# Optimization experiments

Measured on AMD Instinct MI355X. Metric: run time of the kernel, lower is better.

Reference implementation:

```python
import jax, jax.numpy as jnp
import numpy as np

D, H1, O, E = 1024, 4096, 1024, 8
B = 8192


def setup_inputs() -> dict:
    key = jax.random.key(0)
    k1, k2, k3, k4 = jax.random.split(key, 4)
    # kaiming_uniform_ with nonlinearity='relu': bound = sqrt(6 / fan_in), fan_in = last dim
    b_w1 = float(np.sqrt(6.0 / D))
    b_w2 = float(np.sqrt(6.0 / H1))
    x = jax.random.normal(k1, (B, D), dtype=jnp.float32)
    eid = jax.random.randint(k2, (B,), 0, E, dtype=jnp.int32)
    W1 = jax.random.uniform(k3, (E, H1, D), dtype=jnp.float32, minval=-b_w1, maxval=b_w1)
    W2 = jax.random.uniform(k4, (E, O, H1), dtype=jnp.float32, minval=-b_w2, maxval=b_w2)
    b2 = jnp.zeros((E, O), dtype=jnp.float32)
    return {"x": x, "eid": eid, "W1": W1, "W2": W2, "b2": b2}


def reference(x, eid, W1, W2, b2):
    # Per-token expert MLP: y_i = gelu(x_i @ W1[eid_i].T) @ W2[eid_i].T + b2[eid_i]
    # Dense-dispatch formulation: loop over the (small, static) expert axis,
    # compute each expert MLP on all tokens, and select per-token via mask.
    # Math is identical to the sort/gather/scatter original.
    y = jnp.zeros((x.shape[0], W2.shape[1]), dtype=x.dtype)
    for e in range(W1.shape[0]):
        h = jax.nn.gelu(x @ W1[e].T, approximate=False)   # [B, H1]
        y_e = h @ W2[e].T + b2[e]                          # [B, O]
        mask = (eid == e)[:, None].astype(x.dtype)
        y = y + mask * y_e
    return y
```

## Files before the change

### kernel.cpp

```cpp
#include <hip/hip_runtime.h>
#include <hip/hip_bf16.h>
#include <math.h>

constexpr int kD  = 1024;
constexpr int kH1 = 4096;
constexpr int kO  = 1024;
constexpr int kE  = 8;
constexpr int kB  = 8192;

constexpr int BM   = 128;
constexpr int MAXT = kB / BM + kE;

typedef __attribute__((ext_vector_type(8))) short short8;
typedef __attribute__((ext_vector_type(4))) float f32x4;

__device__ __forceinline__ unsigned short f2bf(float f) {
  unsigned int u = __float_as_uint(f);
  u += 0x7fffu + ((u >> 16) & 1u);
  return (unsigned short)(u >> 16);
}
__device__ __forceinline__ float bf2f(unsigned short u) {
  return __uint_as_float(((unsigned int)u) << 16);
}

__device__ __forceinline__ float gelu_fast(float x) {
  float u = 0.7978845608028654f * (x + 0.044715f * x * x * x);
  float eu = __expf(2.0f * u);
  float th = 1.0f - 2.0f / (eu + 1.0f);
  return 0.5f * x * (1.0f + th);
}

__global__ __launch_bounds__(256) void setup_kernel(const int* __restrict__ eid,
                                                    int* __restrict__ perm,
                                                    int* __restrict__ tiles) {
  __shared__ int cnt[kE];
  __shared__ int off[kE];
  __shared__ int cur[kE];
  int t = threadIdx.x;
  if (t < kE) { cnt[t] = 0; cur[t] = 0; }
  __syncthreads();
  for (int i = t; i < kB; i += 256) atomicAdd(&cnt[eid[i]], 1);
  __syncthreads();
  if (t == 0) {
    int o = 0, nt = 0;
    for (int e = 0; e < kE; ++e) {
      off[e] = o;
      int c = cnt[e];
      for (int r = 0; r < c; r += BM) {
        tiles[nt * 4 + 0] = e;
        tiles[nt * 4 + 1] = o + r;
        tiles[nt * 4 + 2] = (c - r < BM) ? (c - r) : BM;
        tiles[nt * 4 + 3] = 0;
        ++nt;
      }
      o += c;
    }
    for (; nt < MAXT; ++nt) {
      tiles[nt * 4 + 0] = 0; tiles[nt * 4 + 1] = 0;
      tiles[nt * 4 + 2] = 0; tiles[nt * 4 + 3] = 0;
    }
  }
  __syncthreads();
  for (int i = t; i < kB; i += 256) {
    int e = eid[i];
    int p = off[e] + atomicAdd(&cur[e], 1);
    perm[p] = i;
  }
}

__global__ __launch_bounds__(256) void gather_kernel(const float* __restrict__ x,
                                                     const int* __restrict__ perm,
                                                     unsigned short* __restrict__ xg) {
  int idx = blockIdx.x * 256 + threadIdx.x;
  int pos = idx >> 7;
  int c   = (idx & 127) << 3;
  int row = perm[pos];
  const float4* s = (const float4*)(x + (size_t)row * kD + c);
  float4 f0 = s[0], f1 = s[1];
  short8 v;
  v[0] = (short)f2bf(f0.x); v[1] = (short)f2bf(f0.y);
  v[2] = (short)f2bf(f0.z); v[3] = (short)f2bf(f0.w);
  v[4] = (short)f2bf(f1.x); v[5] = (short)f2bf(f1.y);
  v[6] = (short)f2bf(f1.z); v[7] = (short)f2bf(f1.w);
  *(short8*)(xg + (size_t)pos * kD + c) = v;
}

__global__ __launch_bounds__(256) void convert_kernel(const float* __restrict__ src,
                                                      unsigned short* __restrict__ dst,
                                                      int n8) {
  int stride = gridDim.x * 256;
  for (int i = blockIdx.x * 256 + threadIdx.x; i < n8; i += stride) {
    const float4* s = (const float4*)(src + (size_t)i * 8);
    float4 f0 = s[0], f1 = s[1];
    short8 v;
    v[0] = (short)f2bf(f0.x); v[1] = (short)f2bf(f0.y);
    v[2] = (short)f2bf(f0.z); v[3] = (short)f2bf(f0.w);
    v[4] = (short)f2bf(f1.x); v[5] = (short)f2bf(f1.y);
    v[6] = (short)f2bf(f1.z); v[7] = (short)f2bf(f1.w);
    *(short8*)(dst + (size_t)i * 8) = v;
  }
}

template <int KTOT, int KTILES, int N, int NPAN, int MODE>
__global__ __launch_bounds__(512, 2) void gemm2p_kernel(
    const unsigned short* __restrict__ Amat,
    const unsigned short* __restrict__ Bmat,
    const int* __restrict__ tiles,
    const int* __restrict__ perm,
    unsigned short* __restrict__ out_bf,
    float* __restrict__ out_f) {
  extern __shared__ unsigned short lds[];

  constexpr int total = MAXT * NPAN;
  constexpr int cpx = total >> 3;
  constexpr int nchN = NPAN / 4;
  const int bid = blockIdx.x;
  const int id = (bid & 7) * cpx + (bid >> 3);
  const int chunk = id >> 4;
  const int a16 = id & 15;
  const int ti = (chunk / nchN) * 4 + (a16 & 3);
  const int pancol = (chunk % nchN) * 4 + (a16 >> 2);

  int n0, kb, half;
  if constexpr (MODE == 0) {
    n0 = pancol * 256; kb = 0; half = 0;
  } else {
    half = pancol >> 2; n0 = (pancol & 3) * 256; kb = half * (KTOT / 2);
  }

  const int e  = tiles[ti * 4 + 0];
  const int rs = tiles[ti * 4 + 1];
  const int nr = tiles[ti * 4 + 2];
  if (nr == 0) return;

  const int t = threadIdx.x;
  const int l = t & 63;
  const int w = t >> 6;
  const int r0 = (w >> 2) * 64;
  const int wc16 = (w & 3) * 16;

  const unsigned short* Bp = Bmat + (size_t)e * N * KTOT;

  int offA[4][2], offB[4][2];
#pragma unroll
  for (int mr = 0; mr < 4; ++mr)
#pragma unroll
    for (int ks = 0; ks < 2; ++ks) {
      int r = r0 + mr * 16 + (l & 15);
      offA[mr][ks] = r * 64 + ((ks * 32 + (l >> 4) * 8) ^ ((r & 7) << 3));
    }
#pragma unroll
  for (int j = 0; j < 4; ++j)
#pragma unroll
    for (int ks = 0; ks < 2; ++ks) {
      int rB = 64 * (j & 1) + wc16 + (l & 15);
      offB[j][ks] = (j >> 1) * 8192 + rB * 64 +
                    ((ks * 32 + (l >> 4) * 8) ^ ((rB & 7) << 3));
    }

  auto stage = [&](int buf, int k0, int idx) {
    const int slot = idx >> 1, hf = idx & 1;
    int elem = (hf * 512 + t) * 8;
    int r = elem >> 6, cp = elem & 63;
    int cl = cp ^ ((r & 7) << 3);
    const unsigned short* src =
        (slot == 0) ? Amat + (size_t)(rs + r) * KTOT + k0 + cl
                    : Bp + (size_t)(n0 + (slot - 1) * 128 + r) * KTOT + k0 + cl;
    unsigned short* dst = lds + buf * 24576 + slot * 8192 + elem;
    __builtin_amdgcn_global_load_lds(
        (const __attribute__((address_space(1))) unsigned int*)src,
        (__attribute__((address_space(3))) unsigned int*)dst, 16, 0, 0);
  };

  short8 aF[4][2], bF[4][2];
  f32x4 acc[4][4] = {};

  auto readA = [&](int buf) {
    const unsigned short* base = lds + buf * 24576;
#pragma unroll
    for (int mr = 0; mr < 4; ++mr)
#pragma unroll
      for (int ks = 0; ks < 2; ++ks)
        aF[mr][ks] = *(const short8*)(base + offA[mr][ks]);
  };
  auto readB = [&](int buf, int jlo) {
    const unsigned short* base = lds + buf * 24576 + 8192;
#pragma unroll
    for (int j = 0; j < 2; ++j)
#pragma unroll
      for (int ks = 0; ks < 2; ++ks)
        bF[jlo + j][ks] = *(const short8*)(base + offB[jlo + j][ks]);
  };
  auto mfmaH = [&](int jlo) {
    __builtin_amdgcn_s_setprio(1);
#pragma unroll
    for (int j = 0; j < 2; ++j)
#pragma unroll
      for (int mr = 0; mr < 4; ++mr)
#pragma unroll
        for (int ks = 0; ks < 2; ++ks)
          acc[jlo + j][mr] = __builtin_amdgcn_mfma_f32_16x16x32_bf16(
              aF[mr][ks], bF[jlo + j][ks], acc[jlo + j][mr], 0, 0, 0);
    __builtin_amdgcn_s_setprio(0);
  };

#pragma unroll
  for (int idx = 0; idx < 6; ++idx) stage(0, kb, idx);

  for (int kt = 0; kt < KTILES - 1; ++kt) {
    const int buf = kt & 1;
    const int nb = buf ^ 1;
    const int k0n = kb + (kt + 1) * 64;
    asm volatile("s_waitcnt vmcnt(2)" ::: "memory");
    __builtin_amdgcn_s_barrier();
    readA(buf);
    readB(buf, 0);
    stage(nb, k0n, 0); stage(nb, k0n, 1); stage(nb, k0n, 2);
    __builtin_amdgcn_s_barrier();
    mfmaH(0);
    asm volatile("s_waitcnt vmcnt(3)" ::: "memory");
    __builtin_amdgcn_s_barrier();
    readB(buf, 2);
    stage(nb, k0n, 3); stage(nb, k0n, 4); stage(nb, k0n, 5);
    __builtin_amdgcn_s_barrier();
    mfmaH(2);
  }
  {
    const int buf = (KTILES - 1) & 1;
    asm volatile("s_waitcnt vmcnt(2)" ::: "memory");
    __builtin_amdgcn_s_barrier();
    readA(buf);
    readB(buf, 0);
    __builtin_amdgcn_s_barrier();
    mfmaH(0);
    asm volatile("s_waitcnt vmcnt(0)" ::: "memory");
    __builtin_amdgcn_s_barrier();
    readB(buf, 2);
    __builtin_amdgcn_s_barrier();
    mfmaH(2);
  }

  const int lr4 = (l >> 4) * 4;
  const int lc  = l & 15;
#pragma unroll
  for (int mr = 0; mr < 4; ++mr)
#pragma unroll
    for (int rg = 0; rg < 4; ++rg) {
      int row = r0 + mr * 16 + lr4 + rg;
      if (row < nr) {
        if constexpr (MODE == 0) {
          unsigned short* dst = out_bf + (size_t)(rs + row) * N + n0;
#pragma unroll
          for (int j = 0; j < 4; ++j)
            dst[j * 64 + wc16 + lc] = f2bf(gelu_fast(acc[j][mr][rg]));
        } else {
          if (half == 0) {
            float* dst = out_f + (size_t)perm[rs + row] * N + n0;
#pragma unroll
            for (int j = 0; j < 4; ++j)
              dst[j * 64 + wc16 + lc] = acc[j][mr][rg];
          } else {
            unsigned short* dst = out_bf + (size_t)(rs + row) * N + n0;
#pragma unroll
            for (int j = 0; j < 4; ++j)
              dst[j * 64 + wc16 + lc] = f2bf(acc[j][mr][rg]);
          }
        }
      }
    }
}

__global__ __launch_bounds__(256) void reduce_kernel(float* __restrict__ y,
                                                     const unsigned short* __restrict__ part,
                                                     const int* __restrict__ perm,
                                                     const int* __restrict__ eid,
                                                     const float* __restrict__ b2) {
  int idx = blockIdx.x * 256 + threadIdx.x;
  int p = idx >> 7;
  int c = (idx & 127) << 3;
  int orig = perm[p];
  int e = eid[orig];
  float* yp = y + (size_t)orig * kO + c;
  short8 pv = *(const short8*)(part + (size_t)p * kO + c);
  const float* bp = b2 + (size_t)e * kO + c;
  float4 y0 = *(float4*)yp, y1 = *(float4*)(yp + 4);
  float4 b0 = *(const float4*)bp, b1 = *(const float4*)(bp + 4);
  y0.x += bf2f((unsigned short)pv[0]) + b0.x;
  y0.y += bf2f((unsigned short)pv[1]) + b0.y;
  y0.z += bf2f((unsigned short)pv[2]) + b0.z;
  y0.w += bf2f((unsigned short)pv[3]) + b0.w;
  y1.x += bf2f((unsigned short)pv[4]) + b1.x;
  y1.y += bf2f((unsigned short)pv[5]) + b1.y;
  y1.z += bf2f((unsigned short)pv[6]) + b1.z;
  y1.w += bf2f((unsigned short)pv[7]) + b1.w;
  *(float4*)yp = y0;
  *(float4*)(yp + 4) = y1;
}

extern "C" void kernel_launch(void* const* d_in, const int* in_sizes, int n_in,
                              void* d_out, int out_size, void* d_ws, size_t ws_size,
                              hipStream_t stream) {
  const float* x  = (const float*)d_in[0];
  const int*  eid = (const int*)d_in[1];
  const float* W1 = (const float*)d_in[2];
  const float* W2 = (const float*)d_in[3];
  const float* b2 = (const float*)d_in[4];
  float* y = (float*)d_out;

  char* ws = (char*)d_ws;
  int* perm  = (int*)ws;
  int* tiles = (int*)(ws + 32768);
  unsigned short* xg = (unsigned short*)(ws + 36864);
  size_t xg_bytes = (size_t)(kB + 256) * kD * 2;
  unsigned short* h  = (unsigned short*)(ws + 36864 + xg_bytes);
  size_t h_bytes = (size_t)(kB + 256) * kH1 * 2;
  unsigned short* Wb = (unsigned short*)(ws + 36864 + xg_bytes + h_bytes);

  constexpr int kWelems8 = kE * kH1 * kD / 8;

  auto g1 = gemm2p_kernel<kD, 16, kH1, 16, 0>;
  auto g2 = gemm2p_kernel<kH1, 32, kO, 8, 1>;
  hipFuncSetAttribute((const void*)g1, hipFuncAttributeMaxDynamicSharedMemorySize, 98304);
  hipFuncSetAttribute((const void*)g2, hipFuncAttributeMaxDynamicSharedMemorySize, 98304);

  setup_kernel<<<1, 256, 0, stream>>>(eid, perm, tiles);
  gather_kernel<<<(kB * kD / 8) / 256, 256, 0, stream>>>(x, perm, xg);

  convert_kernel<<<2048, 256, 0, stream>>>(W1, Wb, kWelems8);
  g1<<<MAXT * 16, 512, 98304, stream>>>(xg, Wb, tiles, perm, h, nullptr);

  convert_kernel<<<2048, 256, 0, stream>>>(W2, Wb, kWelems8);
  g2<<<MAXT * 8, 512, 98304, stream>>>(h, Wb, tiles, perm, xg, y);

  reduce_kernel<<<(kB * kO / 8) / 256, 256, 0, stream>>>(y, xg, perm, eid, b2);
}
```

Baseline: 340.4 us.

## Make expert GEMMs persistent with cross-tile prefetch of next tile's operands

Both grouped GEMM launches become persistent kernels on a fixed grid of 256 workgroups. Each workgroup loops over tiles with a stride of 256. During the last K-step of the current tile it stages the first K-slice of the next tile, so the load pipeline stays busy across tile boundaries and the per-block prologue is paid once per workgroup. In exchange, only one workgroup per CU is resident even though the launch bounds allow two. Empty padding tiles no longer exit early and run the full MMA loop, and tile counts that are not a multiple of 256 can leave a ragged tail.

```diff
diff --git a/kernel.cpp b/kernel.cpp
--- a/kernel.cpp
+++ b/kernel.cpp
@@ -102,7 +102,7 @@
 }
 
 template <int KTOT, int KTILES, int N, int NPAN, int MODE>
-__global__ __launch_bounds__(512, 2) void gemm2p_kernel(
+__global__ __launch_bounds__(512, 2) void gemmp_kernel(
     const unsigned short* __restrict__ Amat,
     const unsigned short* __restrict__ Bmat,
     const int* __restrict__ tiles,
@@ -110,36 +110,41 @@
     unsigned short* __restrict__ out_bf,
     float* __restrict__ out_f) {
   extern __shared__ unsigned short lds[];
-
-  constexpr int total = MAXT * NPAN;
-  constexpr int cpx = total >> 3;
-  constexpr int nchN = NPAN / 4;
+  constexpr int TOTAL = MAXT * NPAN;
+  constexpr int nchN = NPAN / 4 > 0 ? NPAN / 4 : 1;
+
   const int bid = blockIdx.x;
-  const int id = (bid & 7) * cpx + (bid >> 3);
-  const int chunk = id >> 4;
-  const int a16 = id & 15;
-  const int ti = (chunk / nchN) * 4 + (a16 & 3);
-  const int pancol = (chunk % nchN) * 4 + (a16 >> 2);
-
-  int n0, kb, half;
-  if constexpr (MODE == 0) {
-    n0 = pancol * 256; kb = 0; half = 0;
-  } else {
-    half = pancol >> 2; n0 = (pancol & 3) * 256; kb = half * (KTOT / 2);
-  }
-
-  const int e  = tiles[ti * 4 + 0];
-  const int rs = tiles[ti * 4 + 1];
-  const int nr = tiles[ti * 4 + 2];
-  if (nr == 0) return;
-
   const int t = threadIdx.x;
   const int l = t & 63;
   const int w = t >> 6;
   const int r0 = (w >> 2) * 64;
   const int wc16 = (w & 3) * 16;
 
-  const unsigned short* Bp = Bmat + (size_t)e * N * KTOT;
+  struct TP {
+    const unsigned short* Ab;
+    const unsigned short* Bb;
+    int rs, nr, n0, half;
+  };
+
+  auto mkTP = [&](int wg) {
+    TP p;
+    int id = (wg & 7) * (TOTAL / 8) + (wg >> 3);
+    int chunk = id >> 4, a16 = id & 15;
+    int ti = (chunk / nchN) * 4 + (a16 & 3);
+    int pancol = (chunk % nchN) * 4 + (a16 >> 2);
+    int kb;
+    if constexpr (MODE == 0) {
+      p.n0 = pancol * 256; kb = 0; p.half = 0;
+    } else {
+      p.half = pancol >> 2; p.n0 = (pancol & 3) * 256; kb = p.half * (KTOT / 2);
+    }
+    int e = tiles[ti * 4 + 0];
+    p.rs = tiles[ti * 4 + 1];
+    p.nr = tiles[ti * 4 + 2];
+    p.Ab = Amat + (size_t)p.rs * KTOT + kb;
+    p.Bb = Bmat + ((size_t)e * N + p.n0) * KTOT + kb;
+    return p;
+  };
 
   int offA[4][2], offB[4][2];
 #pragma unroll
@@ -158,14 +163,14 @@
                     ((ks * 32 + (l >> 4) * 8) ^ ((rB & 7) << 3));
     }
 
-  auto stage = [&](int buf, int k0, int idx) {
+  auto stageT = [&](const TP& p, int k0, int buf, int idx) {
     const int slot = idx >> 1, hf = idx & 1;
     int elem = (hf * 512 + t) * 8;
     int r = elem >> 6, cp = elem & 63;
     int cl = cp ^ ((r & 7) << 3);
     const unsigned short* src =
-        (slot == 0) ? Amat + (size_t)(rs + r) * KTOT + k0 + cl
-                    : Bp + (size_t)(n0 + (slot - 1) * 128 + r) * KTOT + k0 + cl;
+        (slot == 0) ? p.Ab + (size_t)r * KTOT + k0 + cl
+                    : p.Bb + (size_t)((slot - 1) * 128 + r) * KTOT + k0 + cl;
     unsigned short* dst = lds + buf * 24576 + slot * 8192 + elem;
     __builtin_amdgcn_global_load_lds(
         (const __attribute__((address_space(1))) unsigned int*)src,
@@ -204,70 +209,82 @@
     __builtin_amdgcn_s_setprio(0);
   };
 
-#pragma unroll
-  for (int idx = 0; idx < 6; ++idx) stage(0, kb, idx);
-
-  for (int kt = 0; kt < KTILES - 1; ++kt) {
-    const int buf = kt & 1;
-    const int nb = buf ^ 1;
-    const int k0n = kb + (kt + 1) * 64;
-    asm volatile("s_waitcnt vmcnt(2)" ::: "memory");
-    __builtin_amdgcn_s_barrier();
-    readA(buf);
-    readB(buf, 0);
-    stage(nb, k0n, 0); stage(nb, k0n, 1); stage(nb, k0n, 2);
-    __builtin_amdgcn_s_barrier();
-    mfmaH(0);
-    asm volatile("s_waitcnt vmcnt(3)" ::: "memory");
-    __builtin_amdgcn_s_barrier();
-    readB(buf, 2);
-    stage(nb, k0n, 3); stage(nb, k0n, 4); stage(nb, k0n, 5);
-    __builtin_amdgcn_s_barrier();
-    mfmaH(2);
-  }
-  {
-    const int buf = (KTILES - 1) & 1;
-    asm volatile("s_waitcnt vmcnt(2)" ::: "memory");
-    __builtin_amdgcn_s_barrier();
-    readA(buf);
-    readB(buf, 0);
-    __builtin_amdgcn_s_barrier();
-    mfmaH(0);
-    asm volatile("s_waitcnt vmcnt(0)" ::: "memory");
-    __builtin_amdgcn_s_barrier();
-    readB(buf, 2);
-    __builtin_amdgcn_s_barrier();
-    mfmaH(2);
-  }
-
   const int lr4 = (l >> 4) * 4;
   const int lc  = l & 15;
-#pragma unroll
-  for (int mr = 0; mr < 4; ++mr)
-#pragma unroll
-    for (int rg = 0; rg < 4; ++rg) {
-      int row = r0 + mr * 16 + lr4 + rg;
-      if (row < nr) {
-        if constexpr (MODE == 0) {
-          unsigned short* dst = out_bf + (size_t)(rs + row) * N + n0;
-#pragma unroll
-          for (int j = 0; j < 4; ++j)
-            dst[j * 64 + wc16 + lc] = f2bf(gelu_fast(acc[j][mr][rg]));
-        } else {
-          if (half == 0) {
-            float* dst = out_f + (size_t)perm[rs + row] * N + n0;
+  auto epilogue = [&](const TP& p) {
+#pragma unroll
+    for (int mr = 0; mr < 4; ++mr)
+#pragma unroll
+      for (int rg = 0; rg < 4; ++rg) {
+        int row = r0 + mr * 16 + lr4 + rg;
+        if (row < p.nr) {
+          if constexpr (MODE == 0) {
+            unsigned short* dst = out_bf + (size_t)(p.rs + row) * N + p.n0;
 #pragma unroll
             for (int j = 0; j < 4; ++j)
-              dst[j * 64 + wc16 + lc] = acc[j][mr][rg];
+              dst[j * 64 + wc16 + lc] = f2bf(gelu_fast(acc[j][mr][rg]));
           } else {
-            unsigned short* dst = out_bf + (size_t)(rs + row) * N + n0;
-#pragma unroll
-            for (int j = 0; j < 4; ++j)
-              dst[j * 64 + wc16 + lc] = f2bf(acc[j][mr][rg]);
+            if (p.half == 0) {
+              float* dst = out_f + (size_t)perm[p.rs + row] * N + p.n0;
+#pragma unroll
+              for (int j = 0; j < 4; ++j)
+                dst[j * 64 + wc16 + lc] = acc[j][mr][rg];
+            } else {
+              unsigned short* dst = out_bf + (size_t)(p.rs + row) * N + p.n0;
+#pragma unroll
+              for (int j = 0; j < 4; ++j)
+                dst[j * 64 + wc16 + lc] = f2bf(acc[j][mr][rg]);
+            }
           }
         }
       }
-    }
+  };
+
+  const int nt = (TOTAL - 1 - bid) / 256 + 1;
+  int wg = bid;
+  TP cur = mkTP(wg);
+  int parity = 0;
+
+#pragma unroll
+  for (int idx = 0; idx < 6; ++idx) stageT(cur, 0, 0, idx);
+
+#pragma unroll 1
+  for (int it = 0; it < nt; ++it) {
+    const bool lastT = (it == nt - 1);
+    TP nxt = lastT ? cur : mkTP(wg + 256);
+#pragma unroll 1
+    for (int kt = 0; kt < KTILES; ++kt) {
+      const int buf = parity;
+      const int nb = buf ^ 1;
+      parity = nb;
+      const bool cross = (kt == KTILES - 1);
+      const bool lastV = lastT && cross;
+      const TP& sp = cross ? nxt : cur;
+      const int k0s = cross ? 0 : (kt + 1) * 64;
+      asm volatile("s_waitcnt vmcnt(2)" ::: "memory");
+      __builtin_amdgcn_s_barrier();
+      readA(buf);
+      readB(buf, 0);
+      if (!lastV) { stageT(sp, k0s, nb, 0); stageT(sp, k0s, nb, 1); stageT(sp, k0s, nb, 2); }
+      __builtin_amdgcn_s_barrier();
+      mfmaH(0);
+      if (!lastV) asm volatile("s_waitcnt vmcnt(3)" ::: "memory");
+      else        asm volatile("s_waitcnt vmcnt(0)" ::: "memory");
+      __builtin_amdgcn_s_barrier();
+      readB(buf, 2);
+      if (!lastV) { stageT(sp, k0s, nb, 3); stageT(sp, k0s, nb, 4); stageT(sp, k0s, nb, 5); }
+      __builtin_amdgcn_s_barrier();
+      mfmaH(2);
+    }
+    epilogue(cur);
+#pragma unroll
+    for (int j = 0; j < 4; ++j)
+#pragma unroll
+      for (int mr = 0; mr < 4; ++mr)
+        acc[j][mr] = (f32x4){0.f, 0.f, 0.f, 0.f};
+    cur = nxt;
+    wg += 256;
+  }
 }
 
 __global__ __launch_bounds__(256) void reduce_kernel(float* __restrict__ y,
@@ -318,8 +335,8 @@
 
   constexpr int kWelems8 = kE * kH1 * kD / 8;
 
-  auto g1 = gemm2p_kernel<kD, 16, kH1, 16, 0>;
-  auto g2 = gemm2p_kernel<kH1, 32, kO, 8, 1>;
+  auto g1 = gemmp_kernel<kD, 16, kH1, 16, 0>;
+  auto g2 = gemmp_kernel<kH1, 32, kO, 8, 1>;
   hipFuncSetAttribute((const void*)g1, hipFuncAttributeMaxDynamicSharedMemorySize, 98304);
   hipFuncSetAttribute((const void*)g2, hipFuncAttributeMaxDynamicSharedMemorySize, 98304);
 
@@ -327,10 +344,10 @@
   gather_kernel<<<(kB * kD / 8) / 256, 256, 0, stream>>>(x, perm, xg);
 
   convert_kernel<<<2048, 256, 0, stream>>>(W1, Wb, kWelems8);
-  g1<<<MAXT * 16, 512, 98304, stream>>>(xg, Wb, tiles, perm, h, nullptr);
+  g1<<<256, 512, 98304, stream>>>(xg, Wb, tiles, perm, h, nullptr);
 
   convert_kernel<<<2048, 256, 0, stream>>>(W2, Wb, kWelems8);
-  g2<<<MAXT * 8, 512, 98304, stream>>>(h, Wb, tiles, perm, xg, y);
+  g2<<<256, 512, 98304, stream>>>(h, Wb, tiles, perm, xg, y);
 
   reduce_kernel<<<(kB * kO / 8) / 256, 256, 0, stream>>>(y, xg, perm, eid, b2);
 }
```

New measurement: 356.8 us. 4.8% more time.

## Fuse fp32-to-bf16 weight conversion into GEMM with triple-buffered fp32 LDS staging

Applied to the files above, without the earlier changes.

Removes the two separate weight-conversion kernels and has each GEMM load fp32 weights directly into LDS, converting them to bf16 in registers just before the MFMAs. The k-tile shrinks to 32, staging becomes a three-buffer pipeline in 120KB of LDS, and occupancy drops to one block per CU. This saves a full write and re-read of the bf16 weight copies. In exchange, each GEMM block re-reads fp32 weights at twice the bytes, converts them redundantly across row tiles, and issues more LDS traffic per MFMA.

```diff
diff --git a/kernel.cpp b/kernel.cpp
--- a/kernel.cpp
+++ b/kernel.cpp
@@ -28,6 +28,11 @@
   float eu = __expf(2.0f * u);
   float th = 1.0f - 2.0f / (eu + 1.0f);
   return 0.5f * x * (1.0f + th);
+}
+
+__device__ __forceinline__ unsigned int pk2(float a, float b) {
+  __hip_bfloat162 h = __float22bfloat162_rn(make_float2(a, b));
+  return *reinterpret_cast<unsigned int*>(&h);
 }
 
 __global__ __launch_bounds__(256) void setup_kernel(const int* __restrict__ eid,
@@ -85,37 +90,20 @@
   *(short8*)(xg + (size_t)pos * kD + c) = v;
 }
 
-__global__ __launch_bounds__(256) void convert_kernel(const float* __restrict__ src,
-                                                      unsigned short* __restrict__ dst,
-                                                      int n8) {
-  int stride = gridDim.x * 256;
-  for (int i = blockIdx.x * 256 + threadIdx.x; i < n8; i += stride) {
-    const float4* s = (const float4*)(src + (size_t)i * 8);
-    float4 f0 = s[0], f1 = s[1];
-    short8 v;
-    v[0] = (short)f2bf(f0.x); v[1] = (short)f2bf(f0.y);
-    v[2] = (short)f2bf(f0.z); v[3] = (short)f2bf(f0.w);
-    v[4] = (short)f2bf(f1.x); v[5] = (short)f2bf(f1.y);
-    v[6] = (short)f2bf(f1.z); v[7] = (short)f2bf(f1.w);
-    *(short8*)(dst + (size_t)i * 8) = v;
-  }
-}
-
 template <int KTOT, int KTILES, int N, int NPAN, int MODE>
-__global__ __launch_bounds__(512, 2) void gemm2p_kernel(
+__global__ __launch_bounds__(512, 1) void gemmf_kernel(
     const unsigned short* __restrict__ Amat,
-    const unsigned short* __restrict__ Bmat,
+    const float* __restrict__ Wmat,
     const int* __restrict__ tiles,
     const int* __restrict__ perm,
     unsigned short* __restrict__ out_bf,
     float* __restrict__ out_f) {
-  extern __shared__ unsigned short lds[];
-
-  constexpr int total = MAXT * NPAN;
-  constexpr int cpx = total >> 3;
-  constexpr int nchN = NPAN / 4;
+  extern __shared__ char lds[];
+  constexpr int TOTAL = MAXT * NPAN;
+  constexpr int nchN = NPAN / 4 > 0 ? NPAN / 4 : 1;
+
   const int bid = blockIdx.x;
-  const int id = (bid & 7) * cpx + (bid >> 3);
+  const int id = (bid & 7) * (TOTAL / 8) + (bid >> 3);
   const int chunk = id >> 4;
   const int a16 = id & 15;
   const int ti = (chunk / nchN) * 4 + (a16 & 3);
@@ -139,105 +127,98 @@
   const int r0 = (w >> 2) * 64;
   const int wc16 = (w & 3) * 16;
 
-  const unsigned short* Bp = Bmat + (size_t)e * N * KTOT;
-
-  int offA[4][2], offB[4][2];
-#pragma unroll
-  for (int mr = 0; mr < 4; ++mr)
-#pragma unroll
-    for (int ks = 0; ks < 2; ++ks) {
-      int r = r0 + mr * 16 + (l & 15);
-      offA[mr][ks] = r * 64 + ((ks * 32 + (l >> 4) * 8) ^ ((r & 7) << 3));
-    }
-#pragma unroll
-  for (int j = 0; j < 4; ++j)
-#pragma unroll
-    for (int ks = 0; ks < 2; ++ks) {
-      int rB = 64 * (j & 1) + wc16 + (l & 15);
-      offB[j][ks] = (j >> 1) * 8192 + rB * 64 +
-                    ((ks * 32 + (l >> 4) * 8) ^ ((rB & 7) << 3));
-    }
-
-  auto stage = [&](int buf, int k0, int idx) {
-    const int slot = idx >> 1, hf = idx & 1;
-    int elem = (hf * 512 + t) * 8;
-    int r = elem >> 6, cp = elem & 63;
-    int cl = cp ^ ((r & 7) << 3);
-    const unsigned short* src =
-        (slot == 0) ? Amat + (size_t)(rs + r) * KTOT + k0 + cl
-                    : Bp + (size_t)(n0 + (slot - 1) * 128 + r) * KTOT + k0 + cl;
-    unsigned short* dst = lds + buf * 24576 + slot * 8192 + elem;
+  const unsigned short* Ab = Amat + (size_t)rs * KTOT + kb;
+  const float* Bb = Wmat + ((size_t)e * N + n0) * KTOT + kb;
+
+  const int s_rr = t >> 3, s_c8 = t & 7;
+  const int s_v = s_c8 ^ (s_rr & 7);
+  const size_t aSrc = (size_t)(s_rr * 2 + (s_v >> 2)) * KTOT + (s_v & 3) * 8;
+  const int bRow = t >> 3;
+  const int bLs4 = ((t & 7) ^ ((t >> 3) & 7)) * 4;
+
+  int offA[4];
+#pragma unroll
+  for (int mr = 0; mr < 4; ++mr) {
+    int r = r0 + mr * 16 + (l & 15);
+    int g = l >> 4;
+    int rr = r >> 1;
+    int c8 = (((r & 1) << 2) | g) ^ (rr & 7);
+    offA[mr] = rr * 64 + c8 * 8;
+  }
+  int offB[4][2];
+#pragma unroll
+  for (int j = 0; j < 4; ++j) {
+    int rB = j * 64 + wc16 + (l & 15);
+    int g = l >> 4;
+#pragma unroll
+    for (int h = 0; h < 2; ++h) {
+      int s = (g * 2 + h) ^ (rB & 7);
+      offB[j][h] = rB * 32 + s * 4;
+    }
+  }
+
+  auto stage = [&](int buf, int k0) {
+    char* base = lds + buf * 40960;
     __builtin_amdgcn_global_load_lds(
-        (const __attribute__((address_space(1))) unsigned int*)src,
-        (__attribute__((address_space(3))) unsigned int*)dst, 16, 0, 0);
+        (const __attribute__((address_space(1))) unsigned int*)(Ab + aSrc + k0),
+        (__attribute__((address_space(3))) unsigned int*)(base + t * 16), 16, 0, 0);
+#pragma unroll
+    for (int i = 0; i < 4; ++i) {
+      const float* src = Bb + (size_t)(i * 64 + bRow) * KTOT + k0 + bLs4;
+      __builtin_amdgcn_global_load_lds(
+          (const __attribute__((address_space(1))) unsigned int*)src,
+          (__attribute__((address_space(3))) unsigned int*)(base + 8192 + (i * 512 + t) * 16),
+          16, 0, 0);
+    }
   };
 
-  short8 aF[4][2], bF[4][2];
   f32x4 acc[4][4] = {};
 
-  auto readA = [&](int buf) {
-    const unsigned short* base = lds + buf * 24576;
+  stage(0, kb - kb + 0);
+  stage(1, 32);
+
+  int bcur = 0;
+#pragma unroll 1
+  for (int kt = 0; kt < KTILES; ++kt) {
+    if (kt == KTILES - 1) asm volatile("s_waitcnt vmcnt(0)" ::: "memory");
+    else                  asm volatile("s_waitcnt vmcnt(5)" ::: "memory");
+    __builtin_amdgcn_s_barrier();
+    char* base = lds + bcur * 40960;
+    const unsigned short* As = (const unsigned short*)base;
+    const float* Bs = (const float*)(base + 8192);
+    short8 aF[4];
 #pragma unroll
     for (int mr = 0; mr < 4; ++mr)
-#pragma unroll
-      for (int ks = 0; ks < 2; ++ks)
-        aF[mr][ks] = *(const short8*)(base + offA[mr][ks]);
-  };
-  auto readB = [&](int buf, int jlo) {
-    const unsigned short* base = lds + buf * 24576 + 8192;
-#pragma unroll
-    for (int j = 0; j < 2; ++j)
-#pragma unroll
-      for (int ks = 0; ks < 2; ++ks)
-        bF[jlo + j][ks] = *(const short8*)(base + offB[jlo + j][ks]);
-  };
-  auto mfmaH = [&](int jlo) {
+      aF[mr] = *(const short8*)(As + offA[mr]);
+    float4 bFf[4][2];
+#pragma unroll
+    for (int j = 0; j < 4; ++j) {
+      bFf[j][0] = *(const float4*)(Bs + offB[j][0]);
+      bFf[j][1] = *(const float4*)(Bs + offB[j][1]);
+    }
+    if (kt < KTILES - 2) {
+      int bst = bcur + 2; if (bst >= 3) bst -= 3;
+      stage(bst, (kt + 2) * 32);
+    }
+    short8 bF[4];
+#pragma unroll
+    for (int j = 0; j < 4; ++j) {
+      union { unsigned int u[4]; short8 v; } un;
+      un.u[0] = pk2(bFf[j][0].x, bFf[j][0].y);
+      un.u[1] = pk2(bFf[j][0].z, bFf[j][0].w);
+      un.u[2] = pk2(bFf[j][1].x, bFf[j][1].y);
+      un.u[3] = pk2(bFf[j][1].z, bFf[j][1].w);
+      bF[j] = un.v;
+    }
     __builtin_amdgcn_s_setprio(1);
 #pragma unroll
-    for (int j = 0; j < 2; ++j)
+    for (int j = 0; j < 4; ++j)
 #pragma unroll
       for (int mr = 0; mr < 4; ++mr)
-#pragma unroll
-        for (int ks = 0; ks < 2; ++ks)
-          acc[jlo + j][mr] = __builtin_amdgcn_mfma_f32_16x16x32_bf16(
-              aF[mr][ks], bF[jlo + j][ks], acc[jlo + j][mr], 0, 0, 0);
+        acc[j][mr] = __builtin_amdgcn_mfma_f32_16x16x32_bf16(
+            aF[mr], bF[j], acc[j][mr], 0, 0, 0);
     __builtin_amdgcn_s_setprio(0);
-  };
-
-#pragma unroll
-  for (int idx = 0; idx < 6; ++idx) stage(0, kb, idx);
-
-  for (int kt = 0; kt < KTILES - 1; ++kt) {
-    const int buf = kt & 1;
-    const int nb = buf ^ 1;
-    const int k0n = kb + (kt + 1) * 64;
-    asm volatile("s_waitcnt vmcnt(2)" ::: "memory");
-    __builtin_amdgcn_s_barrier();
-    readA(buf);
-    readB(buf, 0);
-    stage(nb, k0n, 0); stage(nb, k0n, 1); stage(nb, k0n, 2);
-    __builtin_amdgcn_s_barrier();
-    mfmaH(0);
-    asm volatile("s_waitcnt vmcnt(3)" ::: "memory");
-    __builtin_amdgcn_s_barrier();
-    readB(buf, 2);
-    stage(nb, k0n, 3); stage(nb, k0n, 4); stage(nb, k0n, 5);
-    __builtin_amdgcn_s_barrier();
-    mfmaH(2);
-  }
-  {
-    const int buf = (KTILES - 1) & 1;
-    asm volatile("s_waitcnt vmcnt(2)" ::: "memory");
-    __builtin_amdgcn_s_barrier();
-    readA(buf);
-    readB(buf, 0);
-    __builtin_amdgcn_s_barrier();
-    mfmaH(0);
-    asm volatile("s_waitcnt vmcnt(0)" ::: "memory");
-    __builtin_amdgcn_s_barrier();
-    readB(buf, 2);
-    __builtin_amdgcn_s_barrier();
-    mfmaH(2);
+    ++bcur; if (bcur >= 3) bcur = 0;
   }
 
   const int lr4 = (l >> 4) * 4;
@@ -313,24 +294,18 @@
   unsigned short* xg = (unsigned short*)(ws + 36864);
   size_t xg_bytes = (size_t)(kB + 256) * kD * 2;
   unsigned short* h  = (unsigned short*)(ws + 36864 + xg_bytes);
-  size_t h_bytes = (size_t)(kB + 256) * kH1 * 2;
-  unsigned short* Wb = (unsigned short*)(ws + 36864 + xg_bytes + h_bytes);
-
-  constexpr int kWelems8 = kE * kH1 * kD / 8;
-
-  auto g1 = gemm2p_kernel<kD, 16, kH1, 16, 0>;
-  auto g2 = gemm2p_kernel<kH1, 32, kO, 8, 1>;
-  hipFuncSetAttribute((const void*)g1, hipFuncAttributeMaxDynamicSharedMemorySize, 98304);
-  hipFuncSetAttribute((const void*)g2, hipFuncAttributeMaxDynamicSharedMemorySize, 98304);
+
+  auto g1 = gemmf_kernel<kD, 32, kH1, 16, 0>;
+  auto g2 = gemmf_kernel<kH1, 64, kO, 8, 1>;
+  hipFuncSetAttribute((const void*)g1, hipFuncAttributeMaxDynamicSharedMemorySize, 122880);
+  hipFuncSetAttribute((const void*)g2, hipFuncAttributeMaxDynamicSharedMemorySize, 122880);
 
   setup_kernel<<<1, 256, 0, stream>>>(eid, perm, tiles);
   gather_kernel<<<(kB * kD / 8) / 256, 256, 0, stream>>>(x, perm, xg);
 
-  convert_kernel<<<2048, 256, 0, stream>>>(W1, Wb, kWelems8);
-  g1<<<MAXT * 16, 512, 98304, stream>>>(xg, Wb, tiles, perm, h, nullptr);
-
-  convert_kernel<<<2048, 256, 0, stream>>>(W2, Wb, kWelems8);
-  g2<<<MAXT * 8, 512, 98304, stream>>>(h, Wb, tiles, perm, xg, y);
+  g1<<<MAXT * 16, 512, 122880, stream>>>(xg, W1, tiles, perm, h, nullptr);
+
+  g2<<<MAXT * 8, 512, 122880, stream>>>(h, W2, tiles, perm, xg, y);
 
   reduce_kernel<<<(kB * kO / 8) / 256, 256, 0, stream>>>(y, xg, perm, eid, b2);
 }
```

Result: slower. 387.1 us (+13.7%).
